# Kernel tuning notes

Hardware: AMD Instinct MI355X
Metric: run time of the kernel (lower is better)

Reference implementation:

```python
import jax, jax.numpy as jnp
import numpy as np

INIT_W = 0.1  # init_weight uniform range


def setup_inputs() -> dict:
    key = jax.random.key(0)
    kq, kk, kwq, kwk, ka = jax.random.split(key, 5)
    B, b, t_q, t_k = 2, 16, 64, 128
    qs = ks = nu = 512
    query = jax.random.normal(kq, (B, b, t_q, qs), dtype=jnp.float32)
    keys = jax.random.normal(kk, (B, b, t_k, ks), dtype=jnp.float32)
    # torch Linear weight layout: (out_features, in_features), per fusion slice
    Wq = (jax.random.uniform(kwq, (B, nu, qs), dtype=jnp.float32) * 2 - 1) * INIT_W
    Wk = (jax.random.uniform(kwk, (B, nu, ks), dtype=jnp.float32) * 2 - 1) * INIT_W
    linear_att = (jax.random.uniform(ka, (nu,), dtype=jnp.float32) * 2 - 1) * INIT_W
    return {"query": query, "keys": keys, "Wq": Wq, "Wk": Wk, "linear_att": linear_att}


def reference(query, keys, Wq, Wk, linear_att):
    # query: (B, b, t_q, query_size), keys: (B, b, t_k, key_size)
    # HFTA-fused linear projections (no bias): y = x @ W.T per fusion slice
    pq = jnp.einsum('Bbqi,Boi->Bbqo', query, Wq)   # (B, b, t_q, n)
    pk = jnp.einsum('Bbki,Boi->Bbko', keys, Wk)    # (B, b, t_k, n)
    # Bahdanau additive score: tanh(q + k) . v  (broadcast add over t_q x t_k)
    sum_qk = pq[:, :, :, None, :] + pk[:, :, None, :, :]   # (B, b, t_q, t_k, n)
    scores = jnp.einsum('Bbqkn,n->Bbqk', jnp.tanh(sum_qk), linear_att)
    scores_normalized = jax.nn.softmax(scores, axis=-1)    # (B, b, t_q, t_k)
    # context uses RAW keys (not projected)
    context = jnp.einsum('Bbqk,Bbkn->Bbqn', scores_normalized, keys)
    return context, scores_normalized
```

## Files before the change

### kernel.cpp

```cpp
#include <hip/hip_runtime.h>


#define DEV_INLINE __device__ __forceinline__

constexpr float C2    = 2.8853900817779268f;
constexpr float LOG2E = 1.4426950408889634f;

typedef _Float16 f16x8 __attribute__((ext_vector_type(8)));
typedef float    f32x16 __attribute__((ext_vector_type(16)));

DEV_INLINE unsigned int pk2(float a, float b) {
    auto h = __builtin_amdgcn_cvt_pkrtz(a, b);
    return __builtin_bit_cast(unsigned int, h);
}

#define GL2LDS16(g, l) __builtin_amdgcn_global_load_lds( \
    (const __attribute__((address_space(1))) void*)(g),  \
    (__attribute__((address_space(3))) void*)(l), 16, 0, 0)

__global__ __launch_bounds__(256)
void cvt_f16_kernel(const float* __restrict__ query, const float* __restrict__ keys,
                    const float* __restrict__ Wq,    const float* __restrict__ Wk,
                    uint2* __restrict__ dst)
{
    const int i4 = blockIdx.x * 256 + threadIdx.x;
    const float* src; int base;
    if (i4 < 262144)      { src = query; base = 0; }
    else if (i4 < 786432) { src = keys;  base = 262144; }
    else if (i4 < 917504) { src = Wq;    base = 786432; }
    else                  { src = Wk;    base = 917504; }
    const float4 v = *reinterpret_cast<const float4*>(src + (size_t)(i4 - base) * 4);
    dst[i4] = make_uint2(pk2(v.x, v.y), pk2(v.z, v.w));
}

__global__ __launch_bounds__(256)
void proj_mfma_kernel(const _Float16* __restrict__ X16,
                      float* __restrict__ pqT, float* __restrict__ pkT)
{
    __shared__ __align__(16) unsigned char smem[24576];

    const int bid = (blockIdx.x & 7) * 48 + (blockIdx.x >> 3);

    int Bi, mt, tt, tkshift;
    const _Float16 *Wb, *Xb; float* Y;
    if (bid < 128) {
        Bi = bid >> 6; mt = (bid >> 4) & 3; tt = bid & 15;
        Xb = X16 + ((size_t)Bi * 1024 + tt * 64) * 512;
        Wb = X16 + 3145728 + (size_t)Bi * 262144 + (size_t)(mt * 128) * 512;
        Y = pqT; tkshift = 6;
    } else {
        const int b2 = bid - 128;
        Bi = b2 >> 7; mt = (b2 >> 5) & 3; tt = b2 & 31;
        Xb = X16 + 1048576 + ((size_t)Bi * 2048 + tt * 64) * 512;
        Wb = X16 + 3670016 + (size_t)Bi * 262144 + (size_t)(mt * 128) * 512;
        Y = pkT; tkshift = 7;
    }
    const int tid = threadIdx.x;

    auto srcoff = [](int u) {
        const int row = u >> 2, s = (u & 3) ^ ((row >> 1) & 3);
        return (size_t)row * 512 + s * 8;
    };
    const _Float16* gA0 = Wb + srcoff(tid);
    const _Float16* gA1 = Wb + srcoff(tid + 256);
    const _Float16* gB  = Xb + srcoff(tid);
    unsigned char* const ldsA0 = smem + tid * 16;
    unsigned char* const ldsA1 = smem + 4096 + tid * 16;
    unsigned char* const ldsB  = smem + 8192 + tid * 16;

    const int wid = tid >> 6, lane = tid & 63;
    const int wm = wid >> 1, wn = wid & 1;
    const int r31 = lane & 31, h = lane >> 5;
    auto lofs = [](int row, int slot) {
        return row * 64 + ((slot ^ ((row >> 1) & 3)) * 16);
    };
    const int rowA0 = wm * 64 + r31, rowA1 = rowA0 + 32, rowB = wn * 32 + r31;
    const int a00 = lofs(rowA0, h),     a01 = lofs(rowA0, 2 + h);
    const int a10 = lofs(rowA1, h),     a11 = lofs(rowA1, 2 + h);
    const int b0  = 8192 + lofs(rowB, h), b1 = 8192 + lofs(rowB, 2 + h);

    f32x16 acc0, acc1;
#pragma unroll
    for (int i = 0; i < 16; ++i) { acc0[i] = 0.f; acc1[i] = 0.f; }

    GL2LDS16(gA0, ldsA0);
    GL2LDS16(gA1, ldsA1);
    GL2LDS16(gB,  ldsB);
    asm volatile("s_waitcnt vmcnt(0)" ::: "memory");
    __builtin_amdgcn_s_barrier();

    for (int ks = 0; ks < 16; ++ks) {
        const int buf = ks & 1;
        if (ks < 15) {
            const int ko = (ks + 1) * 32, bo = (buf ^ 1) * 12288;
            GL2LDS16(gA0 + ko, ldsA0 + bo);
            GL2LDS16(gA1 + ko, ldsA1 + bo);
            GL2LDS16(gB  + ko, ldsB  + bo);
        }
        const unsigned char* sb = smem + buf * 12288;
        const f16x8 fa00 = *reinterpret_cast<const f16x8*>(sb + a00);
        const f16x8 fa01 = *reinterpret_cast<const f16x8*>(sb + a01);
        const f16x8 fa10 = *reinterpret_cast<const f16x8*>(sb + a10);
        const f16x8 fa11 = *reinterpret_cast<const f16x8*>(sb + a11);
        const f16x8 fb0  = *reinterpret_cast<const f16x8*>(sb + b0);
        const f16x8 fb1  = *reinterpret_cast<const f16x8*>(sb + b1);
        acc0 = __builtin_amdgcn_mfma_f32_32x32x16_f16(fa00, fb0, acc0, 0, 0, 0);
        acc0 = __builtin_amdgcn_mfma_f32_32x32x16_f16(fa01, fb1, acc0, 0, 0, 0);
        acc1 = __builtin_amdgcn_mfma_f32_32x32x16_f16(fa10, fb0, acc1, 0, 0, 0);
        acc1 = __builtin_amdgcn_mfma_f32_32x32x16_f16(fa11, fb1, acc1, 0, 0, 0);
        if (ks < 15) {
            asm volatile("s_waitcnt vmcnt(0)" ::: "memory");
            __builtin_amdgcn_s_barrier();
        }
    }

    const int TK = 1 << tkshift;
    const int trow = tt * 64 + wn * 32 + r31;
    const int slice = Bi * 16 + (trow >> tkshift);
    const int t = trow & (TK - 1);
    const int nf0 = mt * 128 + wm * 64 + 4 * h;
#pragma unroll
    for (int ab = 0; ab < 2; ++ab) {
        const f32x16 acc = ab ? acc1 : acc0;
#pragma unroll
        for (int reg = 0; reg < 16; ++reg) {
            const int nf = nf0 + ab * 32 + (reg & 3) + 8 * (reg >> 2);
            Y[((size_t)(slice * 512 + nf) << tkshift) + t] = acc[reg] * C2;
        }
    }
}

DEV_INLINE float wave_rmax(float v) {
#pragma unroll
    for (int off = 32; off; off >>= 1) v = fmaxf(v, __shfl_xor(v, off, 64));
    return v;
}
DEV_INLINE float wave_rsum(float v) {
#pragma unroll
    for (int off = 32; off; off >>= 1) v += __shfl_xor(v, off, 64);
    return v;
}

__global__ __launch_bounds__(512)
void score_ctx_kernel(const float* __restrict__ pqT,
                      const float* __restrict__ pkT,
                      const float* __restrict__ vatt,
                      const float* __restrict__ keys,
                      float* __restrict__ sc_out,
                      float* __restrict__ ctx)
{
    const int xcd = blockIdx.x & 7, ix = blockIdx.x >> 3;
    const int slice = xcd * 4 + (ix >> 4);
    const int q0    = (ix & 15) * 4;
    const int tid   = threadIdx.x;
    const int k     = tid & 127;
    const int nh    = tid >> 7;

    __shared__ __align__(16) float pql[512][4];
    __shared__ float wl[512];
    __shared__ float partial[3][4][128];
    __shared__ __align__(16) float sc[4][128];
    __shared__ float wredm[8], wreds[8], wsum[8];

    {
        const float vv = vatt[tid];
        wl[tid] = -2.f * vv;
        const float4 q4 = *reinterpret_cast<const float4*>(
            pqT + ((size_t)slice * 512 + tid) * 64 + q0);
        *reinterpret_cast<float4*>(&pql[tid][0]) = q4;
        const float s = wave_rsum(vv);
        if ((tid & 63) == 0) wsum[tid >> 6] = s;
    }
    __syncthreads();
    float sumv = 0.f;
#pragma unroll
    for (int w = 0; w < 8; ++w) sumv += wsum[w];

    const float* __restrict__ pkp = pkT + ((size_t)slice * 512 + nh * 128) * 128 + k;
    float a0 = 0.f, a1 = 0.f, a2 = 0.f, a3 = 0.f;
#pragma unroll 4
    for (int n = 0; n < 128; ++n) {
        const float pk = pkp[(size_t)n * 128];
        const float4 pq4 = *reinterpret_cast<const float4*>(&pql[nh * 128 + n][0]);
        const float w = wl[nh * 128 + n];
        const float e0 = __builtin_amdgcn_exp2f(pq4.x + pk);
        const float e1 = __builtin_amdgcn_exp2f(pq4.y + pk);
        const float e2 = __builtin_amdgcn_exp2f(pq4.z + pk);
        const float e3 = __builtin_amdgcn_exp2f(pq4.w + pk);
        a0 = fmaf(w, __builtin_amdgcn_rcpf(e0 + 1.f), a0);
        a1 = fmaf(w, __builtin_amdgcn_rcpf(e1 + 1.f), a1);
        a2 = fmaf(w, __builtin_amdgcn_rcpf(e2 + 1.f), a2);
        a3 = fmaf(w, __builtin_amdgcn_rcpf(e3 + 1.f), a3);
    }
    if (nh) {
        partial[nh - 1][0][k] = a0; partial[nh - 1][1][k] = a1;
        partial[nh - 1][2][k] = a2; partial[nh - 1][3][k] = a3;
    }
    __syncthreads();
    if (!nh) {
        sc[0][k] = a0 + partial[0][0][k] + partial[1][0][k] + partial[2][0][k] + sumv;
        sc[1][k] = a1 + partial[0][1][k] + partial[1][1][k] + partial[2][1][k] + sumv;
        sc[2][k] = a2 + partial[0][2][k] + partial[1][2][k] + partial[2][2][k] + sumv;
        sc[3][k] = a3 + partial[0][3][k] + partial[1][3][k] + partial[2][3][k] + sumv;
    }
    __syncthreads();

    const int j = nh;
    const float orig = sc[j][k];
    float m = wave_rmax(orig);
    if ((tid & 63) == 0) wredm[tid >> 6] = m;
    __syncthreads();
    m = fmaxf(wredm[2 * j], wredm[2 * j + 1]);
    const float e = __builtin_amdgcn_exp2f((orig - m) * LOG2E);
    float s = wave_rsum(e);
    if ((tid & 63) == 0) wreds[tid >> 6] = s;
    __syncthreads();
    s = wreds[2 * j] + wreds[2 * j + 1];
    const float p = e * __builtin_amdgcn_rcpf(s);
    sc_out[((size_t)slice * 64 + q0 + j) * 128 + k] = p;
    sc[j][k] = p;
    __syncthreads();

    const int q = nh, n4 = k;
    const float* __restrict__ kb = keys + (size_t)slice * 65536 + n4 * 4;
    float4 acc = {0.f, 0.f, 0.f, 0.f};
#pragma unroll 2
    for (int k4 = 0; k4 < 32; ++k4) {
        const float4 pv = *reinterpret_cast<const float4*>(&sc[q][k4 * 4]);
        const float4 kv0 = *reinterpret_cast<const float4*>(kb + (size_t)(k4 * 4 + 0) * 512);
        const float4 kv1 = *reinterpret_cast<const float4*>(kb + (size_t)(k4 * 4 + 1) * 512);
        const float4 kv2 = *reinterpret_cast<const float4*>(kb + (size_t)(k4 * 4 + 2) * 512);
        const float4 kv3 = *reinterpret_cast<const float4*>(kb + (size_t)(k4 * 4 + 3) * 512);
        acc.x = fmaf(pv.x, kv0.x, acc.x); acc.y = fmaf(pv.x, kv0.y, acc.y);
        acc.z = fmaf(pv.x, kv0.z, acc.z); acc.w = fmaf(pv.x, kv0.w, acc.w);
        acc.x = fmaf(pv.y, kv1.x, acc.x); acc.y = fmaf(pv.y, kv1.y, acc.y);
        acc.z = fmaf(pv.y, kv1.z, acc.z); acc.w = fmaf(pv.y, kv1.w, acc.w);
        acc.x = fmaf(pv.z, kv2.x, acc.x); acc.y = fmaf(pv.z, kv2.y, acc.y);
        acc.z = fmaf(pv.z, kv2.z, acc.z); acc.w = fmaf(pv.z, kv2.w, acc.w);
        acc.x = fmaf(pv.w, kv3.x, acc.x); acc.y = fmaf(pv.w, kv3.y, acc.y);
        acc.z = fmaf(pv.w, kv3.z, acc.z); acc.w = fmaf(pv.w, kv3.w, acc.w);
    }
    *reinterpret_cast<float4*>(ctx + ((size_t)slice * 64 + q0 + q) * 512 + n4 * 4) = acc;
}

extern "C" void kernel_launch(void* const* d_in, const int* in_sizes, int n_in,
                              void* d_out, int out_size, void* d_ws, size_t ws_size,
                              hipStream_t stream)
{
    const float* query = (const float*)d_in[0];
    const float* keys  = (const float*)d_in[1];
    const float* Wq    = (const float*)d_in[2];
    const float* Wk    = (const float*)d_in[3];
    const float* vatt  = (const float*)d_in[4];

    float* ctx_out = (float*)d_out;
    float* sc_out  = ctx_out + (size_t)32 * 64 * 512;

    float* pqT = (float*)d_ws;
    float* pkT = pqT + (size_t)32 * 512 * 64;
    _Float16* X16 = (_Float16*)((char*)d_ws + 12 * 1024 * 1024);

    cvt_f16_kernel<<<dim3(4096), 256, 0, stream>>>(query, keys, Wq, Wk, (uint2*)X16);
    proj_mfma_kernel<<<dim3(384), 256, 0, stream>>>(X16, pqT, pkT);
    score_ctx_kernel<<<dim3(512), 512, 0, stream>>>(pqT, pkT, vatt, keys, sc_out, ctx_out);
}
```

Measured before the change: 63.38 us.

## Double score/context block to 1024 threads, splitting n and k reductions

The score-context kernel now runs 1024 threads per block instead of 512. The tanh-sum loop over the 512 hidden units is split 8 ways instead of 4, with the partials reduced in shared memory. The context product splits the key dimension in two and combines the halves through shared memory. The intent is to halve per-thread serial work and raise latency hiding, at the cost of more shared memory, extra barriers, idle threads during softmax, and possible register pressure under the 1024-thread launch bound.

```diff
diff --git a/kernel.cpp b/kernel.cpp
--- a/kernel.cpp
+++ b/kernel.cpp
@@ -141,7 +141,7 @@
     return v;
 }
 
-__global__ __launch_bounds__(512)
+__global__ __launch_bounds__(1024)
 void score_ctx_kernel(const float* __restrict__ pqT,
                       const float* __restrict__ pkT,
                       const float* __restrict__ vatt,
@@ -158,11 +158,12 @@
 
     __shared__ __align__(16) float pql[512][4];
     __shared__ float wl[512];
-    __shared__ float partial[3][4][128];
+    __shared__ float partial[7][4][128];
     __shared__ __align__(16) float sc[4][128];
+    __shared__ __align__(16) float4 ctxp[4][128];
     __shared__ float wredm[8], wreds[8], wsum[8];
 
-    {
+    if (tid < 512) {
         const float vv = vatt[tid];
         wl[tid] = -2.f * vv;
         const float4 q4 = *reinterpret_cast<const float4*>(
@@ -176,13 +177,13 @@
 #pragma unroll
     for (int w = 0; w < 8; ++w) sumv += wsum[w];
 
-    const float* __restrict__ pkp = pkT + ((size_t)slice * 512 + nh * 128) * 128 + k;
+    const float* __restrict__ pkp = pkT + ((size_t)slice * 512 + nh * 64) * 128 + k;
     float a0 = 0.f, a1 = 0.f, a2 = 0.f, a3 = 0.f;
 #pragma unroll 4
-    for (int n = 0; n < 128; ++n) {
+    for (int n = 0; n < 64; ++n) {
         const float pk = pkp[(size_t)n * 128];
-        const float4 pq4 = *reinterpret_cast<const float4*>(&pql[nh * 128 + n][0]);
-        const float w = wl[nh * 128 + n];
+        const float4 pq4 = *reinterpret_cast<const float4*>(&pql[nh * 64 + n][0]);
+        const float w = wl[nh * 64 + n];
         const float e0 = __builtin_amdgcn_exp2f(pq4.x + pk);
         const float e1 = __builtin_amdgcn_exp2f(pq4.y + pk);
         const float e2 = __builtin_amdgcn_exp2f(pq4.z + pk);
@@ -198,35 +199,48 @@
     }
     __syncthreads();
     if (!nh) {
-        sc[0][k] = a0 + partial[0][0][k] + partial[1][0][k] + partial[2][0][k] + sumv;
-        sc[1][k] = a1 + partial[0][1][k] + partial[1][1][k] + partial[2][1][k] + sumv;
-        sc[2][k] = a2 + partial[0][2][k] + partial[1][2][k] + partial[2][2][k] + sumv;
-        sc[3][k] = a3 + partial[0][3][k] + partial[1][3][k] + partial[2][3][k] + sumv;
-    }
-    __syncthreads();
-
-    const int j = nh;
-    const float orig = sc[j][k];
-    float m = wave_rmax(orig);
-    if ((tid & 63) == 0) wredm[tid >> 6] = m;
-    __syncthreads();
-    m = fmaxf(wredm[2 * j], wredm[2 * j + 1]);
-    const float e = __builtin_amdgcn_exp2f((orig - m) * LOG2E);
-    float s = wave_rsum(e);
-    if ((tid & 63) == 0) wreds[tid >> 6] = s;
-    __syncthreads();
-    s = wreds[2 * j] + wreds[2 * j + 1];
-    const float p = e * __builtin_amdgcn_rcpf(s);
-    sc_out[((size_t)slice * 64 + q0 + j) * 128 + k] = p;
-    sc[j][k] = p;
-    __syncthreads();
-
-    const int q = nh, n4 = k;
-    const float* __restrict__ kb = keys + (size_t)slice * 65536 + n4 * 4;
+        float s0 = a0 + sumv, s1 = a1 + sumv, s2 = a2 + sumv, s3 = a3 + sumv;
+#pragma unroll
+        for (int p = 0; p < 7; ++p) {
+            s0 += partial[p][0][k]; s1 += partial[p][1][k];
+            s2 += partial[p][2][k]; s3 += partial[p][3][k];
+        }
+        sc[0][k] = s0; sc[1][k] = s1; sc[2][k] = s2; sc[3][k] = s3;
+    }
+    __syncthreads();
+
+    {
+        const int j = nh & 3;
+        float e = 0.f;
+        if (tid < 512) {
+            const float orig = sc[j][k];
+            const float m0 = wave_rmax(orig);
+            if ((tid & 63) == 0) wredm[tid >> 6] = m0;
+            e = orig;
+        }
+        __syncthreads();
+        if (tid < 512) {
+            const float m = fmaxf(wredm[2 * j], wredm[2 * j + 1]);
+            e = __builtin_amdgcn_exp2f((e - m) * LOG2E);
+            const float ss = wave_rsum(e);
+            if ((tid & 63) == 0) wreds[tid >> 6] = ss;
+        }
+        __syncthreads();
+        if (tid < 512) {
+            const float s = wreds[2 * j] + wreds[2 * j + 1];
+            const float p = e * __builtin_amdgcn_rcpf(s);
+            sc_out[((size_t)slice * 64 + q0 + j) * 128 + k] = p;
+            sc[j][k] = p;
+        }
+    }
+    __syncthreads();
+
+    const int q = tid >> 8, n4 = k, ks = (tid >> 7) & 1;
+    const float* __restrict__ kb = keys + (size_t)slice * 65536 + (size_t)ks * 64 * 512 + n4 * 4;
     float4 acc = {0.f, 0.f, 0.f, 0.f};
 #pragma unroll 2
-    for (int k4 = 0; k4 < 32; ++k4) {
-        const float4 pv = *reinterpret_cast<const float4*>(&sc[q][k4 * 4]);
+    for (int k4 = 0; k4 < 16; ++k4) {
+        const float4 pv = *reinterpret_cast<const float4*>(&sc[q][ks * 64 + k4 * 4]);
         const float4 kv0 = *reinterpret_cast<const float4*>(kb + (size_t)(k4 * 4 + 0) * 512);
         const float4 kv1 = *reinterpret_cast<const float4*>(kb + (size_t)(k4 * 4 + 1) * 512);
         const float4 kv2 = *reinterpret_cast<const float4*>(kb + (size_t)(k4 * 4 + 2) * 512);
@@ -240,7 +254,13 @@
         acc.x = fmaf(pv.w, kv3.x, acc.x); acc.y = fmaf(pv.w, kv3.y, acc.y);
         acc.z = fmaf(pv.w, kv3.z, acc.z); acc.w = fmaf(pv.w, kv3.w, acc.w);
     }
-    *reinterpret_cast<float4*>(ctx + ((size_t)slice * 64 + q0 + q) * 512 + n4 * 4) = acc;
+    if (ks) ctxp[q][n4] = acc;
+    __syncthreads();
+    if (!ks) {
+        const float4 o = ctxp[q][n4];
+        acc.x += o.x; acc.y += o.y; acc.z += o.z; acc.w += o.w;
+        *reinterpret_cast<float4*>(ctx + ((size_t)slice * 64 + q0 + q) * 512 + n4 * 4) = acc;
+    }
 }
 
 extern "C" void kernel_launch(void* const* d_in, const int* in_sizes, int n_in,
@@ -262,5 +282,5 @@
 
     cvt_f16_kernel<<<dim3(4096), 256, 0, stream>>>(query, keys, Wq, Wk, (uint2*)X16);
     proj_mfma_kernel<<<dim3(384), 256, 0, stream>>>(X16, pqT, pkT);
-    score_ctx_kernel<<<dim3(512), 512, 0, stream>>>(pqT, pkT, vatt, keys, sc_out, ctx_out);
-}
+    score_ctx_kernel<<<dim3(512), 1024, 0, stream>>>(pqT, pkT, vatt, keys, sc_out, ctx_out);
+}
```

Result: slower. 65.34 us (+3.1%).

## Restructure score kernel around 8-query blocks with LDS-staged, double-buffered pk tiles

Applied to the files above, without the earlier changes.

The score/context kernel now runs 1024 threads per block covering 8 queries. Each thread owns one (query, key) pair and reduces over all 512 features. pk tiles are streamed into LDS with double-buffered global_load_lds, so one load serves 8 queries instead of each thread reading pk from global memory. The projection kernel now writes pq row-major to match this access pattern. The -2*v weight table is precomputed inside the convert kernel, and the constant sum(v) term is dropped because softmax ignores a constant shift. Half of the reciprocals use a Newton-iteration bit trick to offload the transcendental unit. The context matmul reuses each key load across 8 queries and finishes with an LDS tree reduction. This trades far fewer blocks and more LDS and synchronisation for better data reuse.

```diff
diff --git a/kernel.cpp b/kernel.cpp
--- a/kernel.cpp
+++ b/kernel.cpp
@@ -14,15 +14,39 @@
     return __builtin_bit_cast(unsigned int, h);
 }
 
+DEV_INLINE float rcp_nr(float d) {
+    float y = __builtin_bit_cast(float, 0x7EF311C3u - __builtin_bit_cast(unsigned int, d));
+    y = y * (2.0f - d * y);
+    y = y * (2.0f - d * y);
+    return y;
+}
+
 #define GL2LDS16(g, l) __builtin_amdgcn_global_load_lds( \
     (const __attribute__((address_space(1))) void*)(g),  \
     (__attribute__((address_space(3))) void*)(l), 16, 0, 0)
 
+DEV_INLINE float wave_rsum(float v) {
+#pragma unroll
+    for (int off = 32; off; off >>= 1) v += __shfl_xor(v, off, 64);
+    return v;
+}
+DEV_INLINE float wave_rmax(float v) {
+#pragma unroll
+    for (int off = 32; off; off >>= 1) v = fmaxf(v, __shfl_xor(v, off, 64));
+    return v;
+}
+
 __global__ __launch_bounds__(256)
 void cvt_f16_kernel(const float* __restrict__ query, const float* __restrict__ keys,
                     const float* __restrict__ Wq,    const float* __restrict__ Wk,
-                    uint2* __restrict__ dst)
+                    const float* __restrict__ vatt,
+                    uint2* __restrict__ dst, float* __restrict__ wtab)
 {
+    if (blockIdx.x == 4096) {
+        const int t = threadIdx.x;
+        wtab[t] = -2.f * vatt[t]; wtab[t + 256] = -2.f * vatt[t + 256];
+        return;
+    }
     const int i4 = blockIdx.x * 256 + threadIdx.x;
     const float* src; int base;
     if (i4 < 262144)      { src = query; base = 0; }
@@ -41,19 +65,22 @@
 
     const int bid = (blockIdx.x & 7) * 48 + (blockIdx.x >> 3);
 
-    int Bi, mt, tt, tkshift;
-    const _Float16 *Wb, *Xb; float* Y;
+    int Bi, i128, i64;
+    bool qswap;
+    const _Float16 *Ab, *Bb;
     if (bid < 128) {
-        Bi = bid >> 6; mt = (bid >> 4) & 3; tt = bid & 15;
-        Xb = X16 + ((size_t)Bi * 1024 + tt * 64) * 512;
-        Wb = X16 + 3145728 + (size_t)Bi * 262144 + (size_t)(mt * 128) * 512;
-        Y = pqT; tkshift = 6;
+        Bi = bid >> 6; const int r = bid & 63;
+        i128 = r >> 3;
+        i64  = r & 7;
+        Ab = X16 + ((size_t)Bi * 1024 + i128 * 128) * 512;
+        Bb = X16 + 3145728 + (size_t)Bi * 262144 + (size_t)(i64 * 64) * 512;
+        qswap = true;
     } else {
         const int b2 = bid - 128;
-        Bi = b2 >> 7; mt = (b2 >> 5) & 3; tt = b2 & 31;
-        Xb = X16 + 1048576 + ((size_t)Bi * 2048 + tt * 64) * 512;
-        Wb = X16 + 3670016 + (size_t)Bi * 262144 + (size_t)(mt * 128) * 512;
-        Y = pkT; tkshift = 7;
+        Bi = b2 >> 7; i128 = (b2 >> 5) & 3; i64 = b2 & 31;
+        Ab = X16 + 3670016 + (size_t)Bi * 262144 + (size_t)(i128 * 128) * 512;
+        Bb = X16 + 1048576 + ((size_t)Bi * 2048 + i64 * 64) * 512;
+        qswap = false;
     }
     const int tid = threadIdx.x;
 
@@ -61,9 +88,9 @@
         const int row = u >> 2, s = (u & 3) ^ ((row >> 1) & 3);
         return (size_t)row * 512 + s * 8;
     };
-    const _Float16* gA0 = Wb + srcoff(tid);
-    const _Float16* gA1 = Wb + srcoff(tid + 256);
-    const _Float16* gB  = Xb + srcoff(tid);
+    const _Float16* gA0 = Ab + srcoff(tid);
+    const _Float16* gA1 = Ab + srcoff(tid + 256);
+    const _Float16* gB  = Bb + srcoff(tid);
     unsigned char* const ldsA0 = smem + tid * 16;
     unsigned char* const ldsA1 = smem + 4096 + tid * 16;
     unsigned char* const ldsB  = smem + 8192 + tid * 16;
@@ -114,133 +141,169 @@
         }
     }
 
-    const int TK = 1 << tkshift;
-    const int trow = tt * 64 + wn * 32 + r31;
-    const int slice = Bi * 16 + (trow >> tkshift);
-    const int t = trow & (TK - 1);
-    const int nf0 = mt * 128 + wm * 64 + 4 * h;
 #pragma unroll
     for (int ab = 0; ab < 2; ++ab) {
         const f32x16 acc = ab ? acc1 : acc0;
 #pragma unroll
         for (int reg = 0; reg < 16; ++reg) {
-            const int nf = nf0 + ab * 32 + (reg & 3) + 8 * (reg >> 2);
-            Y[((size_t)(slice * 512 + nf) << tkshift) + t] = acc[reg] * C2;
-        }
-    }
-}
-
-DEV_INLINE float wave_rmax(float v) {
-#pragma unroll
-    for (int off = 32; off; off >>= 1) v = fmaxf(v, __shfl_xor(v, off, 64));
-    return v;
-}
-DEV_INLINE float wave_rsum(float v) {
-#pragma unroll
-    for (int off = 32; off; off >>= 1) v += __shfl_xor(v, off, 64);
-    return v;
-}
-
-__global__ __launch_bounds__(512)
+            const int dr = (reg & 3) + 8 * (reg >> 2) + 4 * h;
+            const int arow = wm * 64 + ab * 32 + dr;
+            if (qswap) {
+                const int trow = i128 * 128 + arow;
+                const int n    = i64 * 64 + wn * 32 + r31;
+                const int slice = Bi * 16 + (trow >> 6), t = trow & 63;
+                pqT[((size_t)(slice * 64 + t)) * 512 + n] = acc[reg] * C2;
+            } else {
+                const int nf   = i128 * 128 + arow;
+                const int trow = i64 * 64 + wn * 32 + r31;
+                const int slice = Bi * 16 + (trow >> 7), t = trow & 127;
+                pkT[((size_t)(slice * 512 + nf)) * 128 + t] = acc[reg] * C2;
+            }
+        }
+    }
+}
+
+__global__ __launch_bounds__(1024, 1)
 void score_ctx_kernel(const float* __restrict__ pqT,
                       const float* __restrict__ pkT,
-                      const float* __restrict__ vatt,
+                      const float* __restrict__ wtab,
                       const float* __restrict__ keys,
                       float* __restrict__ sc_out,
                       float* __restrict__ ctx)
 {
-    const int xcd = blockIdx.x & 7, ix = blockIdx.x >> 3;
-    const int slice = xcd * 4 + (ix >> 4);
-    const int q0    = (ix & 15) * 4;
+    const int wg = (blockIdx.x & 7) * 32 + (blockIdx.x >> 3);
+    const int slice = wg >> 3;
+    const int q0    = (wg & 7) * 8;
     const int tid   = threadIdx.x;
+    const int q     = tid >> 7;
     const int k     = tid & 127;
-    const int nh    = tid >> 7;
-
-    __shared__ __align__(16) float pql[512][4];
-    __shared__ float wl[512];
-    __shared__ float partial[3][4][128];
-    __shared__ __align__(16) float sc[4][128];
-    __shared__ float wredm[8], wreds[8], wsum[8];
+
+    __shared__ __align__(16) float pkbuf[2][64][128];
+    __shared__ __align__(16) float pqlq[8][512];
+    __shared__ float scP[8][128];
+    __shared__ float red[16], red2[16];
 
     {
-        const float vv = vatt[tid];
-        wl[tid] = -2.f * vv;
-        const float4 q4 = *reinterpret_cast<const float4*>(
-            pqT + ((size_t)slice * 512 + tid) * 64 + q0);
-        *reinterpret_cast<float4*>(&pql[tid][0]) = q4;
-        const float s = wave_rsum(vv);
-        if ((tid & 63) == 0) wsum[tid >> 6] = s;
-    }
-    __syncthreads();
-    float sumv = 0.f;
-#pragma unroll
-    for (int w = 0; w < 8; ++w) sumv += wsum[w];
-
-    const float* __restrict__ pkp = pkT + ((size_t)slice * 512 + nh * 128) * 128 + k;
-    float a0 = 0.f, a1 = 0.f, a2 = 0.f, a3 = 0.f;
+        const int f = tid * 4, qq = f >> 9, n0 = f & 511;
+        const float4 v = *reinterpret_cast<const float4*>(
+            pqT + ((size_t)(slice * 64 + q0 + qq)) * 512 + n0);
+        *reinterpret_cast<float4*>(&pqlq[qq][n0]) = v;
+    }
+    const float* __restrict__ pkbase = pkT + (size_t)slice * 65536;
+    {
+        unsigned char* d = (unsigned char*)&pkbuf[0][0][0];
+        GL2LDS16(pkbase + (size_t)tid * 4,        d + tid * 16);
+        GL2LDS16(pkbase + 4096 + (size_t)tid * 4, d + 16384 + tid * 16);
+    }
+    __syncthreads();
+
+    float a = 0.f;
+    for (int c = 0; c < 8; ++c) {
+        const int buf = c & 1;
+        if (c < 7) {
+            unsigned char* d = (unsigned char*)&pkbuf[buf ^ 1][0][0];
+            const float* g = pkbase + (size_t)(c + 1) * 8192;
+            GL2LDS16(g + (size_t)tid * 4,        d + tid * 16);
+            GL2LDS16(g + 4096 + (size_t)tid * 4, d + 16384 + tid * 16);
+        }
+#pragma unroll
+        for (int nl4 = 0; nl4 < 16; ++nl4) {
+            const float4 pq4 = *reinterpret_cast<const float4*>(&pqlq[q][c * 64 + nl4 * 4]);
+            const float4 w4  = *reinterpret_cast<const float4*>(&wtab[c * 64 + nl4 * 4]);
+            const float pqa[4] = {pq4.x, pq4.y, pq4.z, pq4.w};
+            const float wa[4]  = {w4.x, w4.y, w4.z, w4.w};
+#pragma unroll
+            for (int j = 0; j < 4; ++j) {
+                const float pk = pkbuf[buf][nl4 * 4 + j][k];
+                const float e  = __builtin_amdgcn_exp2f(pqa[j] + pk) + 1.f;
+                const float r  = (j < 2) ? __builtin_amdgcn_rcpf(e) : rcp_nr(e);
+                a = fmaf(wa[j], r, a);
+            }
+        }
+        if (c < 7) {
+            asm volatile("s_waitcnt vmcnt(0)" ::: "memory");
+            __builtin_amdgcn_s_barrier();
+        }
+    }
+
+    const int wid = tid >> 6;
+    {
+        const float m0 = wave_rmax(a);
+        if ((tid & 63) == 0) red[wid] = m0;
+    }
+    __syncthreads();
+    const float m = fmaxf(red[2 * q], red[2 * q + 1]);
+    float e = __builtin_amdgcn_exp2f((a - m) * LOG2E);
+    {
+        const float s0 = wave_rsum(e);
+        if ((tid & 63) == 0) red2[wid] = s0;
+    }
+    __syncthreads();
+    const float s = red2[2 * q] + red2[2 * q + 1];
+    const float p = e * __builtin_amdgcn_rcpf(s);
+    sc_out[((size_t)(slice * 64 + q0 + q)) * 128 + k] = p;
+    scP[q][k] = p;
+    __syncthreads();
+
+    const int kg = tid >> 7, n4 = tid & 127;
+    float4 acc[8];
+#pragma unroll
+    for (int i = 0; i < 8; ++i) acc[i] = make_float4(0.f, 0.f, 0.f, 0.f);
+    const float* __restrict__ kb = keys + (size_t)slice * 65536 + (size_t)(kg * 16) * 512 + n4 * 4;
 #pragma unroll 4
-    for (int n = 0; n < 128; ++n) {
-        const float pk = pkp[(size_t)n * 128];
-        const float4 pq4 = *reinterpret_cast<const float4*>(&pql[nh * 128 + n][0]);
-        const float w = wl[nh * 128 + n];
-        const float e0 = __builtin_amdgcn_exp2f(pq4.x + pk);
-        const float e1 = __builtin_amdgcn_exp2f(pq4.y + pk);
-        const float e2 = __builtin_amdgcn_exp2f(pq4.z + pk);
-        const float e3 = __builtin_amdgcn_exp2f(pq4.w + pk);
-        a0 = fmaf(w, __builtin_amdgcn_rcpf(e0 + 1.f), a0);
-        a1 = fmaf(w, __builtin_amdgcn_rcpf(e1 + 1.f), a1);
-        a2 = fmaf(w, __builtin_amdgcn_rcpf(e2 + 1.f), a2);
-        a3 = fmaf(w, __builtin_amdgcn_rcpf(e3 + 1.f), a3);
-    }
-    if (nh) {
-        partial[nh - 1][0][k] = a0; partial[nh - 1][1][k] = a1;
-        partial[nh - 1][2][k] = a2; partial[nh - 1][3][k] = a3;
-    }
-    __syncthreads();
-    if (!nh) {
-        sc[0][k] = a0 + partial[0][0][k] + partial[1][0][k] + partial[2][0][k] + sumv;
-        sc[1][k] = a1 + partial[0][1][k] + partial[1][1][k] + partial[2][1][k] + sumv;
-        sc[2][k] = a2 + partial[0][2][k] + partial[1][2][k] + partial[2][2][k] + sumv;
-        sc[3][k] = a3 + partial[0][3][k] + partial[1][3][k] + partial[2][3][k] + sumv;
-    }
-    __syncthreads();
-
-    const int j = nh;
-    const float orig = sc[j][k];
-    float m = wave_rmax(orig);
-    if ((tid & 63) == 0) wredm[tid >> 6] = m;
-    __syncthreads();
-    m = fmaxf(wredm[2 * j], wredm[2 * j + 1]);
-    const float e = __builtin_amdgcn_exp2f((orig - m) * LOG2E);
-    float s = wave_rsum(e);
-    if ((tid & 63) == 0) wreds[tid >> 6] = s;
-    __syncthreads();
-    s = wreds[2 * j] + wreds[2 * j + 1];
-    const float p = e * __builtin_amdgcn_rcpf(s);
-    sc_out[((size_t)slice * 64 + q0 + j) * 128 + k] = p;
-    sc[j][k] = p;
-    __syncthreads();
-
-    const int q = nh, n4 = k;
-    const float* __restrict__ kb = keys + (size_t)slice * 65536 + n4 * 4;
-    float4 acc = {0.f, 0.f, 0.f, 0.f};
-#pragma unroll 2
-    for (int k4 = 0; k4 < 32; ++k4) {
-        const float4 pv = *reinterpret_cast<const float4*>(&sc[q][k4 * 4]);
-        const float4 kv0 = *reinterpret_cast<const float4*>(kb + (size_t)(k4 * 4 + 0) * 512);
-        const float4 kv1 = *reinterpret_cast<const float4*>(kb + (size_t)(k4 * 4 + 1) * 512);
-        const float4 kv2 = *reinterpret_cast<const float4*>(kb + (size_t)(k4 * 4 + 2) * 512);
-        const float4 kv3 = *reinterpret_cast<const float4*>(kb + (size_t)(k4 * 4 + 3) * 512);
-        acc.x = fmaf(pv.x, kv0.x, acc.x); acc.y = fmaf(pv.x, kv0.y, acc.y);
-        acc.z = fmaf(pv.x, kv0.z, acc.z); acc.w = fmaf(pv.x, kv0.w, acc.w);
-        acc.x = fmaf(pv.y, kv1.x, acc.x); acc.y = fmaf(pv.y, kv1.y, acc.y);
-        acc.z = fmaf(pv.y, kv1.z, acc.z); acc.w = fmaf(pv.y, kv1.w, acc.w);
-        acc.x = fmaf(pv.z, kv2.x, acc.x); acc.y = fmaf(pv.z, kv2.y, acc.y);
-        acc.z = fmaf(pv.z, kv2.z, acc.z); acc.w = fmaf(pv.z, kv2.w, acc.w);
-        acc.x = fmaf(pv.w, kv3.x, acc.x); acc.y = fmaf(pv.w, kv3.y, acc.y);
-        acc.z = fmaf(pv.w, kv3.z, acc.z); acc.w = fmaf(pv.w, kv3.w, acc.w);
-    }
-    *reinterpret_cast<float4*>(ctx + ((size_t)slice * 64 + q0 + q) * 512 + n4 * 4) = acc;
+    for (int r = 0; r < 16; ++r) {
+        const float4 kv = *reinterpret_cast<const float4*>(kb + (size_t)r * 512);
+#pragma unroll
+        for (int qq = 0; qq < 8; ++qq) {
+            const float pv = scP[qq][kg * 16 + r];
+            acc[qq].x = fmaf(pv, kv.x, acc[qq].x);
+            acc[qq].y = fmaf(pv, kv.y, acc[qq].y);
+            acc[qq].z = fmaf(pv, kv.z, acc[qq].z);
+            acc[qq].w = fmaf(pv, kv.w, acc[qq].w);
+        }
+    }
+
+    float4* ctxp = reinterpret_cast<float4*>(&pkbuf[0][0][0]);
+    if (kg >= 4) {
+#pragma unroll
+        for (int qq = 0; qq < 8; ++qq) ctxp[((kg - 4) * 8 + qq) * 128 + n4] = acc[qq];
+    }
+    __syncthreads();
+    if (kg < 4) {
+#pragma unroll
+        for (int qq = 0; qq < 8; ++qq) {
+            const float4 o = ctxp[(kg * 8 + qq) * 128 + n4];
+            acc[qq].x += o.x; acc[qq].y += o.y; acc[qq].z += o.z; acc[qq].w += o.w;
+        }
+    }
+    __syncthreads();
+    if (kg == 2 || kg == 3) {
+#pragma unroll
+        for (int qq = 0; qq < 8; ++qq) ctxp[((kg - 2) * 8 + qq) * 128 + n4] = acc[qq];
+    }
+    __syncthreads();
+    if (kg < 2) {
+#pragma unroll
+        for (int qq = 0; qq < 8; ++qq) {
+            const float4 o = ctxp[(kg * 8 + qq) * 128 + n4];
+            acc[qq].x += o.x; acc[qq].y += o.y; acc[qq].z += o.z; acc[qq].w += o.w;
+        }
+    }
+    __syncthreads();
+    if (kg == 1) {
+#pragma unroll
+        for (int qq = 0; qq < 8; ++qq) ctxp[qq * 128 + n4] = acc[qq];
+    }
+    __syncthreads();
+    if (kg == 0) {
+#pragma unroll
+        for (int qq = 0; qq < 8; ++qq) {
+            const float4 o = ctxp[qq * 128 + n4];
+            acc[qq].x += o.x; acc[qq].y += o.y; acc[qq].z += o.z; acc[qq].w += o.w;
+            *reinterpret_cast<float4*>(
+                ctx + ((size_t)(slice * 64 + q0 + qq)) * 512 + n4 * 4) = acc[qq];
+        }
+    }
 }
 
 extern "C" void kernel_launch(void* const* d_in, const int* in_sizes, int n_in,
@@ -257,10 +320,12 @@
     float* sc_out  = ctx_out + (size_t)32 * 64 * 512;
 
     float* pqT = (float*)d_ws;
-    float* pkT = pqT + (size_t)32 * 512 * 64;
+    float* pkT = pqT + (size_t)32 * 64 * 512;
     _Float16* X16 = (_Float16*)((char*)d_ws + 12 * 1024 * 1024);
-
-    cvt_f16_kernel<<<dim3(4096), 256, 0, stream>>>(query, keys, Wq, Wk, (uint2*)X16);
+    float* wtab = (float*)((char*)d_ws + 20 * 1024 * 1024);
+
+    cvt_f16_kernel<<<dim3(4097), 256, 0, stream>>>(query, keys, Wq, Wk, vatt,
+                                                   (uint2*)X16, wtab);
     proj_mfma_kernel<<<dim3(384), 256, 0, stream>>>(X16, pqT, pkT);
-    score_ctx_kernel<<<dim3(512), 512, 0, stream>>>(pqT, pkT, vatt, keys, sc_out, ctx_out);
-}
+    score_ctx_kernel<<<dim3(256), 1024, 0, stream>>>(pqT, pkT, wtab, keys, sc_out, ctx_out);
+}
```

After: 71.53 us. 1.13x slower.
